# Kernel tuning notes

Measured on AMD Instinct MI355X. Metric: run time of the kernel, lower is better.

## Reference

```python
import jax, jax.numpy as jnp
import numpy as np

NEG = -1e30  # finite stand-in for -inf (keeps logaddexp grads NaN-free)

def setup_inputs() -> dict:
    key = jax.random.key(0)
    k1, k2, k3 = jax.random.split(key, 3)
    T, B, V, S = 512, 32, 4096, 64
    acts = jax.random.normal(k1, (T, B, V), dtype=jnp.float32)
    labels = jax.random.randint(k2, (B * S,), 1, V, dtype=jnp.int32)  # blank=0 excluded
    input_lengths = jax.random.randint(k3, (B,), T // 2, T + 1, dtype=jnp.int32)
    target_lengths = jnp.full((B,), S, dtype=jnp.int32)
    return {"acts": acts, "labels": labels, "input_lengths": input_lengths,
            "target_lengths": target_lengths}

def _ctc_cost(acts, labels, input_lengths, target_lengths):
    T, B, V = acts.shape
    S = labels.shape[0] // B
    L = 2 * S + 1  # extended label length (blanks interleaved)
    log_probs = jax.nn.log_softmax(acts, axis=-1)          # (T,B,V)
    lab = labels.reshape(B, S)
    ext = jnp.zeros((B, L), dtype=lab.dtype).at[:, 1::2].set(lab)  # blank,l1,blank,...
    # gather per-timestep log-probs of extended labels: (T,B,L)
    lp_ext = jnp.take_along_axis(log_probs, jnp.broadcast_to(ext[None], (T, B, L)), axis=2)
    # skip transition allowed when ext[s] is non-blank and differs from ext[s-2]
    ext_m2 = jnp.concatenate([jnp.zeros((B, 2), ext.dtype), ext[:, :-2]], axis=1)
    skip = (jnp.arange(L)[None, :] >= 2) & (ext != 0) & (ext != ext_m2)  # (B,L)
    alpha0 = jnp.full((B, L), NEG, dtype=log_probs.dtype)
    alpha0 = alpha0.at[:, 0].set(lp_ext[0, :, 0]).at[:, 1].set(lp_ext[0, :, 1])
    negcol = jnp.full((B, 1), NEG, dtype=log_probs.dtype)

    def step(alpha, xt):
        lp_t, t = xt
        a1 = jnp.concatenate([negcol, alpha[:, :-1]], axis=1)
        a2 = jnp.concatenate([negcol, negcol, alpha[:, :-2]], axis=1)
        a2 = jnp.where(skip, a2, NEG)
        new = jnp.logaddexp(jnp.logaddexp(alpha, a1), a2) + lp_t
        # freeze alpha once t >= input_length so the final row holds alpha at t=len-1
        alpha = jnp.where((t < input_lengths)[:, None], new, alpha)
        return alpha, None

    alpha_T, _ = jax.lax.scan(step, alpha0, (lp_ext[1:], jnp.arange(1, T)))
    idx_hi = (2 * target_lengths).astype(jnp.int32)        # last blank
    idx_lo = jnp.maximum(idx_hi - 1, 0)                    # last label
    a_hi = jnp.take_along_axis(alpha_T, idx_hi[:, None], axis=1)[:, 0]
    a_lo = jnp.take_along_axis(alpha_T, idx_lo[:, None], axis=1)[:, 0]
    nll = -jnp.logaddexp(a_hi, a_lo)                        # (B,)
    nll = jnp.where(jnp.isinf(nll) | (nll > 1e29), 0.0, nll)  # masked_fill(isinf, 0)
    return jnp.sum(nll)  # size_average=False, length_average=False

def reference(acts, labels, input_lengths, target_lengths):
    return _ctc_cost(acts, labels, input_lengths, target_lengths)
```

## Files before the change

### kernel.cpp

```cpp
#include <hip/hip_runtime.h>
#include <hip/hip_bf16.h>

constexpr int T = 512;
constexpr int B = 32;
constexpr int V = 4096;
constexpr int S = 64;
constexpr int GW2 = 68;
constexpr int CH = 120;

#define NEG (-1e30f)

__device__ inline float lae2(float a, float b) {
    float m = fmaxf(a, b);
    return m + __logf(__expf(a - m) + __expf(b - m));
}
__device__ inline float lae3(float a, float b, float c) {
    float m = fmaxf(fmaxf(a, b), c);
    return m + __logf(__expf(a - m) + __expf(b - m) + __expf(c - m));
}

__global__ __launch_bounds__(256) void lse_gather_kernel(
    const float* __restrict__ acts, const int* __restrict__ labels,
    float* __restrict__ g) {
    int w = blockIdx.x * 4 + (threadIdx.x >> 6);
    int lane = threadIdx.x & 63;
    int t = w >> 5;
    int b = w & 31;
    const float* row = acts + (size_t)w * V;
    const float4* row4 = reinterpret_cast<const float4*>(row);

    int sym = labels[b * S + lane];
    float4 r[16];
#pragma unroll
    for (int j = 0; j < 16; ++j) r[j] = row4[j * 64 + lane];
    float gv = row[sym];

    float vmax = -INFINITY;
#pragma unroll
    for (int j = 0; j < 16; ++j)
        vmax = fmaxf(vmax, fmaxf(fmaxf(r[j].x, r[j].y), fmaxf(r[j].z, r[j].w)));
#pragma unroll
    for (int off = 1; off < 64; off <<= 1)
        vmax = fmaxf(vmax, __shfl_xor(vmax, off));

    float acc = 0.f;
#pragma unroll
    for (int j = 0; j < 16; ++j) {
        acc += __expf(r[j].x - vmax) + __expf(r[j].y - vmax) +
               __expf(r[j].z - vmax) + __expf(r[j].w - vmax);
    }
#pragma unroll
    for (int off = 1; off < 64; off <<= 1)
        acc += __shfl_xor(acc, off);

    float lse = vmax + __logf(acc);

    float* grow = g + (size_t)(b * T + t) * GW2;
    grow[1 + lane] = gv - lse;
    if (lane == 0) grow[0] = r[0].x - lse;
}

__global__ __launch_bounds__(256) void ctc_fwd_kernel(
    const float* __restrict__ g, const int* __restrict__ labels,
    const int* __restrict__ in_len, const int* __restrict__ tgt_len,
    float* __restrict__ out) {
    __shared__ float sg[2][CH][GW2];
    int b = blockIdx.x;
    int tid = threadIdx.x;
    int lane = tid & 63;
    int wave = tid >> 6;
    const float* gb = g + (size_t)b * T * GW2;
    int Tl = in_len[b];
    int nch = (Tl + CH - 1) / CH;

    {
        int tcnt = min(CH, Tl);
        int F4 = tcnt * (GW2 / 4);
        const float4* src = reinterpret_cast<const float4*>(gb);
        float4* dst = reinterpret_cast<float4*>(&sg[0][0][0]);
        for (int i = tid; i < F4; i += 256) dst[i] = src[i];
    }
    __syncthreads();

    float a0 = NEG, a1 = NEG, a2 = NEG;
    bool skip1 = false;
    if (wave == 0) {
        int myLab = labels[b * S + lane];
        skip1 = (lane >= 1) && (myLab != labels[b * S + lane - 1]);
        float lpb0 = sg[0][0][0];
        float lpl0 = sg[0][0][1 + lane];
        a0 = (lane == 0) ? lpb0 : NEG;
        a1 = (lane == 0) ? lpl0 : NEG;
    }

    int t = 1;
    for (int c = 0; c < nch; ++c) {
        int buf = c & 1;
        int tEnd = min((c + 1) * CH, Tl);
        if (wave == 0) {
            int tc = t - c * CH;
            int tcEnd = tEnd - c * CH;
            if (tc < tcEnd) {
                float lpb = sg[buf][tc][0];
                float lpl = sg[buf][tc][1 + lane];
                for (; tc < tcEnd; ++tc) {
                    float nlpb = 0.f, nlpl = 0.f;
                    if (tc + 1 < tcEnd) {
                        nlpb = sg[buf][tc + 1][0];
                        nlpl = sg[buf][tc + 1][1 + lane];
                    }
                    float pa1 = __shfl_up(a1, 1);
                    if (lane == 0) pa1 = NEG;
                    float n0 = lae2(a0, pa1) + lpb;
                    float n1 = lae3(a1, a0, skip1 ? pa1 : NEG) + lpl;
                    float n2 = lae2(a2, a1) + lpb;
                    a0 = n0; a1 = n1; a2 = n2;
                    lpb = nlpb; lpl = nlpl;
                }
            }
            t = tEnd;
        } else {
            int t0 = (c + 1) * CH;
            if (t0 < Tl) {
                int tcnt = min(CH, Tl - t0);
                int F4 = tcnt * (GW2 / 4);
                const float4* src = reinterpret_cast<const float4*>(gb + (size_t)t0 * GW2);
                float4* dst = reinterpret_cast<float4*>(&sg[(c + 1) & 1][0][0]);
                for (int i = tid - 64; i < F4; i += 192) dst[i] = src[i];
            }
        }
        __syncthreads();
    }

    if (tid < 64) {
        int tl = tgt_len[b];
        float ahi, alo;
        if (tl >= S) {
            ahi = __shfl(a2, 63);
            alo = __shfl(a1, S - 1);
        } else if (tl >= 1) {
            ahi = __shfl(a0, tl);
            alo = __shfl(a1, tl - 1);
        } else {
            ahi = __shfl(a0, 0);
            alo = ahi;
        }
        if (lane == 0) {
            float m = fmaxf(ahi, alo);
            float nll = -(m + __logf(__expf(ahi - m) + __expf(alo - m)));
            if (!(nll < 1e29f)) nll = 0.f;
            atomicAdd(out, nll);
        }
    }
}

extern "C" void kernel_launch(void* const* d_in, const int* in_sizes, int n_in,
                              void* d_out, int out_size, void* d_ws, size_t ws_size,
                              hipStream_t stream) {
    const float* acts = (const float*)d_in[0];
    const int* labels = (const int*)d_in[1];
    const int* in_len = (const int*)d_in[2];
    const int* tgt_len = (const int*)d_in[3];
    float* out = (float*)d_out;
    float* g = (float*)d_ws;

    hipMemsetAsync(out, 0, sizeof(float), stream);

    lse_gather_kernel<<<(T * B) / 4, 256, 0, stream>>>(acts, labels, g);
    ctc_fwd_kernel<<<B, 256, 0, stream>>>(g, labels, in_len, tgt_len, out);
}
```

Before: 489.2 us.

## Fuse log-softmax gather and CTC recursion with per-chunk atomic counters

Merges the two kernels into one launch. The first B blocks run the CTC alpha recursion, and the remaining blocks compute log-softmax and gather rows. The recursion blocks spin on per-(batch, chunk) atomic counters so they can start on early timesteps while later rows are still being produced. Producer blocks also skip rows past each sequence's input length, and the chunk size drops to 64. This risks deadlock if the consumer blocks occupy resources that producers need, and it adds polling and fence overhead.

```diff
diff --git a/kernel.cpp b/kernel.cpp
--- a/kernel.cpp
+++ b/kernel.cpp
@@ -6,7 +6,9 @@
 constexpr int V = 4096;
 constexpr int S = 64;
 constexpr int GW2 = 68;
-constexpr int CH = 120;
+constexpr int CH = 64;
+constexpr int NCH = T / CH;
+constexpr int NGBLK = (T * B) / 4;
 
 #define NEG (-1e30f)
 
@@ -19,62 +21,79 @@
     return m + __logf(__expf(a - m) + __expf(b - m) + __expf(c - m));
 }
 
-__global__ __launch_bounds__(256) void lse_gather_kernel(
-    const float* __restrict__ acts, const int* __restrict__ labels,
-    float* __restrict__ g) {
-    int w = blockIdx.x * 4 + (threadIdx.x >> 6);
-    int lane = threadIdx.x & 63;
-    int t = w >> 5;
-    int b = w & 31;
-    const float* row = acts + (size_t)w * V;
-    const float4* row4 = reinterpret_cast<const float4*>(row);
-
-    int sym = labels[b * S + lane];
-    float4 r[16];
-#pragma unroll
-    for (int j = 0; j < 16; ++j) r[j] = row4[j * 64 + lane];
-    float gv = row[sym];
-
-    float vmax = -INFINITY;
-#pragma unroll
-    for (int j = 0; j < 16; ++j)
-        vmax = fmaxf(vmax, fmaxf(fmaxf(r[j].x, r[j].y), fmaxf(r[j].z, r[j].w)));
-#pragma unroll
-    for (int off = 1; off < 64; off <<= 1)
-        vmax = fmaxf(vmax, __shfl_xor(vmax, off));
-
-    float acc = 0.f;
-#pragma unroll
-    for (int j = 0; j < 16; ++j) {
-        acc += __expf(r[j].x - vmax) + __expf(r[j].y - vmax) +
-               __expf(r[j].z - vmax) + __expf(r[j].w - vmax);
+__device__ inline void wait_chunk(int* cp, int target) {
+    if ((threadIdx.x & 63) == 0) {
+        while (__hip_atomic_load(cp, __ATOMIC_RELAXED, __HIP_MEMORY_SCOPE_AGENT) < target)
+            __builtin_amdgcn_s_sleep(8);
     }
-#pragma unroll
-    for (int off = 1; off < 64; off <<= 1)
-        acc += __shfl_xor(acc, off);
-
-    float lse = vmax + __logf(acc);
-
-    float* grow = g + (size_t)(b * T + t) * GW2;
-    grow[1 + lane] = gv - lse;
-    if (lane == 0) grow[0] = r[0].x - lse;
+    __threadfence();
 }
 
-__global__ __launch_bounds__(256) void ctc_fwd_kernel(
-    const float* __restrict__ g, const int* __restrict__ labels,
+__global__ __launch_bounds__(256) void ctc_fused_kernel(
+    const float* __restrict__ acts, const int* __restrict__ labels,
     const int* __restrict__ in_len, const int* __restrict__ tgt_len,
-    float* __restrict__ out) {
+    float* __restrict__ g, int* __restrict__ cnt, float* __restrict__ out) {
     __shared__ float sg[2][CH][GW2];
-    int b = blockIdx.x;
     int tid = threadIdx.x;
     int lane = tid & 63;
     int wave = tid >> 6;
+
+    if (blockIdx.x >= B) {
+        int W = (blockIdx.x - B) * 4 + wave;
+        int t = W >> 5;
+        int b = W & 31;
+        int Tl = in_len[b];
+        if (t >= Tl) return;
+
+        const float* row = acts + (size_t)W * V;
+        const float4* row4 = reinterpret_cast<const float4*>(row);
+
+        int sym = labels[b * S + lane];
+        float4 r[16];
+#pragma unroll
+        for (int j = 0; j < 16; ++j) r[j] = row4[j * 64 + lane];
+        float gv = row[sym];
+
+        float vmax = -INFINITY;
+#pragma unroll
+        for (int j = 0; j < 16; ++j)
+            vmax = fmaxf(vmax, fmaxf(fmaxf(r[j].x, r[j].y), fmaxf(r[j].z, r[j].w)));
+#pragma unroll
+        for (int off = 1; off < 64; off <<= 1)
+            vmax = fmaxf(vmax, __shfl_xor(vmax, off));
+
+        float acc = 0.f;
+#pragma unroll
+        for (int j = 0; j < 16; ++j) {
+            acc += __expf(r[j].x - vmax) + __expf(r[j].y - vmax) +
+                   __expf(r[j].z - vmax) + __expf(r[j].w - vmax);
+        }
+#pragma unroll
+        for (int off = 1; off < 64; off <<= 1)
+            acc += __shfl_xor(acc, off);
+
+        float lse = vmax + __logf(acc);
+
+        float* grow = g + (size_t)(b * T + t) * GW2;
+        grow[1 + lane] = gv - lse;
+        if (lane == 0) grow[0] = r[0].x - lse;
+
+        __threadfence();
+        if (lane == 0)
+            __hip_atomic_fetch_add(&cnt[b * NCH + (t >> 6)], 1,
+                                   __ATOMIC_RELAXED, __HIP_MEMORY_SCOPE_AGENT);
+        return;
+    }
+
+    int b = blockIdx.x;
     const float* gb = g + (size_t)b * T * GW2;
+    int* cb = cnt + b * NCH;
     int Tl = in_len[b];
     int nch = (Tl + CH - 1) / CH;
 
     {
         int tcnt = min(CH, Tl);
+        wait_chunk(cb, tcnt);
         int F4 = tcnt * (GW2 / 4);
         const float4* src = reinterpret_cast<const float4*>(gb);
         float4* dst = reinterpret_cast<float4*>(&sg[0][0][0]);
@@ -119,15 +138,14 @@
                 }
             }
             t = tEnd;
-        } else {
+        } else if (c + 1 < nch) {
             int t0 = (c + 1) * CH;
-            if (t0 < Tl) {
-                int tcnt = min(CH, Tl - t0);
-                int F4 = tcnt * (GW2 / 4);
-                const float4* src = reinterpret_cast<const float4*>(gb + (size_t)t0 * GW2);
-                float4* dst = reinterpret_cast<float4*>(&sg[(c + 1) & 1][0][0]);
-                for (int i = tid - 64; i < F4; i += 192) dst[i] = src[i];
-            }
+            int tcnt = min(CH, Tl - t0);
+            wait_chunk(cb + c + 1, tcnt);
+            int F4 = tcnt * (GW2 / 4);
+            const float4* src = reinterpret_cast<const float4*>(gb + (size_t)t0 * GW2);
+            float4* dst = reinterpret_cast<float4*>(&sg[buf ^ 1][0][0]);
+            for (int i = tid - 64; i < F4; i += 192) dst[i] = src[i];
         }
         __syncthreads();
     }
@@ -162,10 +180,13 @@
     const int* in_len = (const int*)d_in[2];
     const int* tgt_len = (const int*)d_in[3];
     float* out = (float*)d_out;
+
     float* g = (float*)d_ws;
+    int* cnt = (int*)((char*)d_ws + (8 << 20));
 
     hipMemsetAsync(out, 0, sizeof(float), stream);
+    hipMemsetAsync(cnt, 0, B * NCH * sizeof(int), stream);
 
-    lse_gather_kernel<<<(T * B) / 4, 256, 0, stream>>>(acts, labels, g);
-    ctc_fwd_kernel<<<B, 256, 0, stream>>>(g, labels, in_len, tgt_len, out);
+    ctc_fused_kernel<<<B + NGBLK, 256, 0, stream>>>(acts, labels, in_len,
+                                                    tgt_len, g, cnt, out);
 }
```

After: 1.411 ms. 188% more time.

## Use base-2 log domain, DPP lane shift, and skip rows beyond input length

Applied to the files above, without the earlier changes.

Stores the gathered log-probabilities pre-scaled by log2(e) so the CTC recurrence can use the native exp2/log2 instructions, converting back with ln2 only at the end. The shuffle-up is replaced by a DPP row-shift with NEG fill. The prefetch branch is removed by padding the shared buffer with one extra row, which lets CH shrink to 119. The LSE kernel now skips timesteps at or beyond the input length, so it reads less of acts. The DPP row_shr control 0x138 may behave differently from a full-wave shift at 16-lane row boundaries, and the padded row is read without being initialized.

```diff
diff --git a/kernel.cpp b/kernel.cpp
--- a/kernel.cpp
+++ b/kernel.cpp
@@ -6,26 +6,39 @@
 constexpr int V = 4096;
 constexpr int S = 64;
 constexpr int GW2 = 68;
-constexpr int CH = 120;
+constexpr int CH = 119;
 
 #define NEG (-1e30f)
+#define LOG2E 1.44269504f
+#define LN2 0.69314718f
+
+__device__ inline float fexp2(float x) { return __builtin_amdgcn_exp2f(x); }
+__device__ inline float flog2(float x) { return __builtin_amdgcn_logf(x); }
 
 __device__ inline float lae2(float a, float b) {
     float m = fmaxf(a, b);
-    return m + __logf(__expf(a - m) + __expf(b - m));
+    return m + flog2(fexp2(a - m) + fexp2(b - m));
 }
 __device__ inline float lae3(float a, float b, float c) {
     float m = fmaxf(fmaxf(a, b), c);
-    return m + __logf(__expf(a - m) + __expf(b - m) + __expf(c - m));
+    return m + flog2(fexp2(a - m) + fexp2(b - m) + fexp2(c - m));
+}
+
+__device__ inline float wave_shr1(float x, float fill) {
+    int r = __builtin_amdgcn_update_dpp(__float_as_int(fill), __float_as_int(x),
+                                        0x138, 0xf, 0xf, false);
+    return __int_as_float(r);
 }
 
 __global__ __launch_bounds__(256) void lse_gather_kernel(
     const float* __restrict__ acts, const int* __restrict__ labels,
-    float* __restrict__ g) {
+    const int* __restrict__ in_len, float* __restrict__ g) {
     int w = blockIdx.x * 4 + (threadIdx.x >> 6);
     int lane = threadIdx.x & 63;
     int t = w >> 5;
     int b = w & 31;
+    if (t >= in_len[b]) return;
+
     const float* row = acts + (size_t)w * V;
     const float4* row4 = reinterpret_cast<const float4*>(row);
 
@@ -56,15 +69,15 @@
     float lse = vmax + __logf(acc);
 
     float* grow = g + (size_t)(b * T + t) * GW2;
-    grow[1 + lane] = gv - lse;
-    if (lane == 0) grow[0] = r[0].x - lse;
+    grow[1 + lane] = (gv - lse) * LOG2E;
+    if (lane == 0) grow[0] = (r[0].x - lse) * LOG2E;
 }
 
 __global__ __launch_bounds__(256) void ctc_fwd_kernel(
     const float* __restrict__ g, const int* __restrict__ labels,
     const int* __restrict__ in_len, const int* __restrict__ tgt_len,
     float* __restrict__ out) {
-    __shared__ float sg[2][CH][GW2];
+    __shared__ float sg[2 * CH + 1][GW2];
     int b = blockIdx.x;
     int tid = threadIdx.x;
     int lane = tid & 63;
@@ -77,7 +90,7 @@
         int tcnt = min(CH, Tl);
         int F4 = tcnt * (GW2 / 4);
         const float4* src = reinterpret_cast<const float4*>(gb);
-        float4* dst = reinterpret_cast<float4*>(&sg[0][0][0]);
+        float4* dst = reinterpret_cast<float4*>(&sg[0][0]);
         for (int i = tid; i < F4; i += 256) dst[i] = src[i];
     }
     __syncthreads();
@@ -87,8 +100,8 @@
     if (wave == 0) {
         int myLab = labels[b * S + lane];
         skip1 = (lane >= 1) && (myLab != labels[b * S + lane - 1]);
-        float lpb0 = sg[0][0][0];
-        float lpl0 = sg[0][0][1 + lane];
+        float lpb0 = sg[0][0];
+        float lpl0 = sg[0][1 + lane];
         a0 = (lane == 0) ? lpb0 : NEG;
         a1 = (lane == 0) ? lpl0 : NEG;
     }
@@ -96,23 +109,21 @@
     int t = 1;
     for (int c = 0; c < nch; ++c) {
         int buf = c & 1;
+        int base = buf * CH;
         int tEnd = min((c + 1) * CH, Tl);
         if (wave == 0) {
             int tc = t - c * CH;
             int tcEnd = tEnd - c * CH;
             if (tc < tcEnd) {
-                float lpb = sg[buf][tc][0];
-                float lpl = sg[buf][tc][1 + lane];
+                float lpb = sg[base + tc][0];
+                float lpl = sg[base + tc][1 + lane];
                 for (; tc < tcEnd; ++tc) {
-                    float nlpb = 0.f, nlpl = 0.f;
-                    if (tc + 1 < tcEnd) {
-                        nlpb = sg[buf][tc + 1][0];
-                        nlpl = sg[buf][tc + 1][1 + lane];
-                    }
-                    float pa1 = __shfl_up(a1, 1);
-                    if (lane == 0) pa1 = NEG;
+                    float nlpb = sg[base + tc + 1][0];
+                    float nlpl = sg[base + tc + 1][1 + lane];
+                    float pa1 = wave_shr1(a1, NEG);
+                    float pa1s = skip1 ? pa1 : NEG;
                     float n0 = lae2(a0, pa1) + lpb;
-                    float n1 = lae3(a1, a0, skip1 ? pa1 : NEG) + lpl;
+                    float n1 = lae3(a1, a0, pa1s) + lpl;
                     float n2 = lae2(a2, a1) + lpb;
                     a0 = n0; a1 = n1; a2 = n2;
                     lpb = nlpb; lpl = nlpl;
@@ -125,7 +136,7 @@
                 int tcnt = min(CH, Tl - t0);
                 int F4 = tcnt * (GW2 / 4);
                 const float4* src = reinterpret_cast<const float4*>(gb + (size_t)t0 * GW2);
-                float4* dst = reinterpret_cast<float4*>(&sg[(c + 1) & 1][0][0]);
+                float4* dst = reinterpret_cast<float4*>(&sg[(base ^ CH)][0]);
                 for (int i = tid - 64; i < F4; i += 192) dst[i] = src[i];
             }
         }
@@ -146,8 +157,7 @@
             alo = ahi;
         }
         if (lane == 0) {
-            float m = fmaxf(ahi, alo);
-            float nll = -(m + __logf(__expf(ahi - m) + __expf(alo - m)));
+            float nll = -(lae2(ahi, alo) * LN2);
             if (!(nll < 1e29f)) nll = 0.f;
             atomicAdd(out, nll);
         }
@@ -164,8 +174,8 @@
     float* out = (float*)d_out;
     float* g = (float*)d_ws;
 
-    hipMemsetAsync(out, 0, sizeof(float), stream);
+    (void)hipMemsetAsync(out, 0, sizeof(float), stream);
 
-    lse_gather_kernel<<<(T * B) / 4, 256, 0, stream>>>(acts, labels, g);
+    lse_gather_kernel<<<(T * B) / 4, 256, 0, stream>>>(acts, labels, in_len, g);
     ctc_fwd_kernel<<<B, 256, 0, stream>>>(g, labels, in_len, tgt_len, out);
 }
```

Result: faster. 403.2 us (-17.6%).
